# Optimization experiments

Measured on AMD Instinct MI355X. Metric: run time of the kernel, lower is better.

## Reference

```python
import jax, jax.numpy as jnp
import numpy as np

EPSILON = 1e-8
MATCH_THRESHOLD = 0.5
MEANINGFUL_RADIUS = 0.05


def setup_inputs() -> dict:
    key = jax.random.key(0)
    ks = jax.random.split(key, 8)
    B, T, H, D, N = 4, 4096, 2048, 256, 8192
    K = H // 4
    s = lambda k, shape, fan_in: jax.random.normal(k, shape, jnp.float32) * (fan_in ** -0.5)
    return {
        "hidden": jax.random.normal(ks[0], (B, T, H), jnp.float32),
        "beliefs": jax.random.normal(ks[1], (N, D), jnp.float32),
        "active_mask": jax.random.bernoulli(ks[2], 0.9, (N,)),
        "W_obs": s(ks[3], (D, H), H),
        "W_g1": s(ks[4], (K, H), H),
        "b_g1": jnp.zeros((K,), jnp.float32),
        "W_g2": s(ks[5], (1, K), K),
        "b_g2": jnp.full((1,), -2.0, jnp.float32),  # nn.init.constant_(bias, -2.0)
        "W_p1": s(ks[6], (K, H), H),
        "b_p1": jnp.zeros((K,), jnp.float32),
        "W_p2": s(ks[7], (1, K), K),
        "b_p2": jnp.zeros((1,), jnp.float32),
    }


def reference(hidden, beliefs, active_mask, W_obs, W_g1, b_g1, W_g2, b_g2, W_p1, b_p1, W_p2, b_p2):
    # --- projections over [B, T, H] ---
    obs = jnp.einsum('bth,dh->btd', hidden, W_obs)                       # [B,T,D]
    g_h = jax.nn.relu(jnp.einsum('bth,kh->btk', hidden, W_g1) + b_g1)
    gate = jax.nn.sigmoid(jnp.einsum('btk,ok->bto', g_h, W_g2) + b_g2)   # [B,T,1]
    p_h = jax.nn.relu(jnp.einsum('bth,kh->btk', hidden, W_p1) + b_p1)
    prec = jax.nn.softplus(jnp.einsum('btk,ok->bto', p_h, W_p2) + b_p2)  # [B,T,1]

    obs_mean = obs.mean(axis=0)            # [T,D]
    prec_mean = (gate * prec).mean(axis=0)  # [T,1]

    # F.normalize(x, dim=-1, eps) == x / max(||x||, eps)
    obs_angles = obs_mean / jnp.maximum(
        jnp.linalg.norm(obs_mean, axis=-1, keepdims=True), EPSILON)
    obs_beliefs = obs_angles * prec_mean    # [T,D], radius = gated precision

    # --- match against active belief slots (fully vectorized, no per-token loop) ---
    obs_r = jnp.linalg.norm(obs_beliefs, axis=-1)                       # [T]
    obs_ang = obs_beliefs / jnp.maximum(obs_r, EPSILON)[:, None]
    bel_r = jnp.maximum(jnp.linalg.norm(beliefs, axis=-1), EPSILON)     # [N]
    bel_ang = beliefs / bel_r[:, None]

    sims = obs_ang @ bel_ang.T              # [T,N] cosine similarities
    neg = jnp.finfo(sims.dtype).min
    masked = jnp.where(active_mask[None, :], sims, neg)
    any_active = jnp.any(active_mask)
    best_sims = jnp.where(any_active, masked.max(axis=-1), 0.0)         # [T]
    best_idx = jnp.where(any_active, jnp.argmax(masked, axis=-1), -1)   # [T]

    meaningful = obs_r > MEANINGFUL_RADIUS
    matched = meaningful & (best_sims > MATCH_THRESHOLD)
    matched_slot = jnp.where(matched, best_idx, -1)                     # -1 == new slot
    match_sim = jnp.where(matched, best_sims, 0.0)

    # vectorized stand-in for list[WriteCandidate]:
    # belief vectors, per-token match similarity, matched slot id, validity mask
    return obs_beliefs, match_sim, matched_slot, meaningful
```

## Files before the change

### kernel.cpp

```cpp
#include <hip/hip_runtime.h>

constexpr int B = 4, T = 4096, H = 2048, D = 256, KK = 512, N = 8192;
constexpr int BT = B * T;
constexpr int NALL = 1280;
constexpr int CAP = 1024;
constexpr int MCAP = 256;

typedef short bf16x8 __attribute__((ext_vector_type(8)));
typedef float f32x4  __attribute__((ext_vector_type(4)));

__device__ __forceinline__ unsigned short f2bf(float f) {
    unsigned u = __float_as_uint(f);
    return (unsigned short)((u + 0x7fffu + ((u >> 16) & 1u)) >> 16);
}
__device__ __forceinline__ float bf2f(unsigned short h) {
    return __uint_as_float((unsigned)h << 16);
}
__device__ __forceinline__ void async16(const void* g, void* l) {
    __builtin_amdgcn_global_load_lds(
        (const __attribute__((address_space(1))) unsigned int*)g,
        (__attribute__((address_space(3))) unsigned int*)l, 16, 0, 0);
}
__device__ __forceinline__ unsigned long long enc_sim(float s, int idx) {
    unsigned bits = __float_as_uint(s);
    unsigned e32 = (bits & 0x80000000u) ? ~bits : (bits | 0x80000000u);
    return ((unsigned long long)e32 << 32) | (unsigned)(~(unsigned)idx);
}
__device__ __forceinline__ unsigned enc_f32(float s) {
    unsigned b = __float_as_uint(s);
    return (b & 0x80000000u) ? ~b : (b | 0x80000000u);
}
__device__ __forceinline__ float dec_f32(unsigned e) {
    return __uint_as_float((e & 0x80000000u) ? (e & 0x7FFFFFFFu) : ~e);
}

constexpr size_t WS_HB   = 0;
constexpr size_t WS_WB   = WS_HB   + (size_t)BT * H * 2;
constexpr size_t WS_BELB = WS_WB   + (size_t)NALL * H * 2;
constexpr size_t WS_OAB  = WS_BELB + (size_t)N * D * 2;
constexpr size_t WS_B1C  = WS_OAB  + (size_t)T * D * 2;
constexpr size_t WS_W2C  = WS_B1C  + 4096;
constexpr size_t WS_FAC  = WS_W2C  + 4096;
constexpr size_t WS_OBSR = WS_FAC  + 16384;
constexpr size_t WS_FLAG = WS_OBSR + 16384;
constexpr size_t WS_ACTV = WS_FLAG + (size_t)CAP * 4;
constexpr size_t WS_META = WS_ACTV + (size_t)N * 4;
constexpr size_t WS_OBS  = WS_META + 256;
constexpr size_t WS_YG   = WS_OBS  + (size_t)T * D * 4;
constexpr size_t WS_YP   = WS_YG   + (size_t)BT * 4;
constexpr size_t WS_ENC  = WS_YP   + (size_t)BT * 4;
constexpr size_t WS_CNT  = WS_ENC  + (size_t)T * 4;
constexpr size_t WS_MCNT = WS_CNT  + 256;
constexpr size_t WS_MLST = WS_MCNT + 256;
constexpr size_t WS_ZEND = WS_MLST + (size_t)MCAP * 4;
constexpr size_t WS_NEEDF = WS_ZEND;
constexpr size_t WS_ZEROSZ = WS_ZEND - WS_OBS;

constexpr int    WTC    = 1280;
constexpr size_t F_WT   = 0;
constexpr size_t F_BEL  = F_WT   + (size_t)H * WTC * 4;
constexpr size_t F_OBS  = F_BEL  + (size_t)N * D * 4;
constexpr size_t F_YG   = F_OBS  + (size_t)T * D * 4;
constexpr size_t F_YP   = F_YG   + (size_t)BT * 4;
constexpr size_t F_OBSR = F_YP   + (size_t)BT * 4;
constexpr size_t F_ENC  = F_OBSR + (size_t)T * 4;
constexpr size_t F_ACT  = F_ENC  + (size_t)T * 8;
constexpr size_t F_META = F_ACT  + (size_t)N * 4;
constexpr size_t F_NEED = F_META + 256;

__global__ void prep_kernel(const float* beliefs, unsigned short* belb,
                            const unsigned char* mask_raw, int* active, int* meta,
                            const float* b_g1, const float* b_p1,
                            const float* W_g2, const float* W_p2,
                            float* b1c, float* w2c) {
    __shared__ int s_f32bad, s_nz_nonaligned;
    int blk = blockIdx.x;
    if (blk < N / 4) {
        int wave = blk * 4 + (threadIdx.x >> 6);
        int lane = threadIdx.x & 63;
        float4 v = ((const float4*)(beliefs + (size_t)wave * D))[lane];
        float ss = v.x * v.x + v.y * v.y + v.z * v.z + v.w * v.w;
        for (int m = 1; m < 64; m <<= 1) ss += __shfl_xor(ss, m, 64);
        float inv = 1.0f / fmaxf(sqrtf(ss), 1e-8f);
        uint2 o;
        o.x = f2bf(v.x * inv) | ((unsigned)f2bf(v.y * inv) << 16);
        o.y = f2bf(v.z * inv) | ((unsigned)f2bf(v.w * inv) << 16);
        *(uint2*)(belb + (size_t)wave * D + lane * 4) = o;
        return;
    }
    if (blk == N / 4) {
        if (threadIdx.x == 0) { s_f32bad = 0; s_nz_nonaligned = 0; }
        __syncthreads();
        const float* rf = (const float*)mask_raw;
        const int*   ri = (const int*)mask_raw;
        for (int i = threadIdx.x; i < N; i += blockDim.x) {
            unsigned char b = mask_raw[i];
            if ((i & 3) && b) atomicOr(&s_nz_nonaligned, 1);
        }
        for (int e = threadIdx.x; e < N / 4; e += blockDim.x) {
            float f = rf[e]; if (!(f == 0.0f || f == 1.0f)) atomicOr(&s_f32bad, 1);
        }
        __syncthreads();
        int layout;
        if (!s_f32bad)            layout = 2;
        else if (s_nz_nonaligned) layout = 1;
        else                      layout = 0;
        for (int n = threadIdx.x; n < N; n += blockDim.x) {
            int a;
            if (layout == 2)      a = (rf[n] != 0.0f);
            else if (layout == 1) a = (mask_raw[n] != 0);
            else                  a = (ri[n] != 0);
            active[n] = a;
        }
        if (threadIdx.x == 0) meta[0] = layout;
        return;
    }
    for (int c = threadIdx.x; c < 1024; c += blockDim.x) {
        if (c < 512) { b1c[c] = b_g1[c];       w2c[c] = W_g2[c]; }
        else         { b1c[c] = b_p1[c - 512]; w2c[c] = W_p2[c - 512]; }
    }
}

__global__ void conv_all(const float* hidden, const float* Wg1, const float* Wp1,
                         const float* Wobs, unsigned short* hb, unsigned short* wb) {
    int blk = blockIdx.x;
    int c8 = threadIdx.x * 8;
    const float* src;
    unsigned short* dst;
    if (blk < BT) {
        src = hidden + (size_t)blk * H;
        dst = hb + (size_t)blk * H;
    } else {
        int row = blk - BT;
        src = (row < 512) ? &Wg1[(size_t)row * H]
            : (row < 1024) ? &Wp1[(size_t)(row - 512) * H]
                           : &Wobs[(size_t)(row - 1024) * H];
        dst = wb + (size_t)row * H;
    }
    float4 v0 = *(const float4*)(src + c8);
    float4 v1 = *(const float4*)(src + c8 + 4);
    uint4 o;
    o.x = f2bf(v0.x) | ((unsigned)f2bf(v0.y) << 16);
    o.y = f2bf(v0.z) | ((unsigned)f2bf(v0.w) << 16);
    o.z = f2bf(v1.x) | ((unsigned)f2bf(v1.y) << 16);
    o.w = f2bf(v1.z) | ((unsigned)f2bf(v1.w) << 16);
    *(uint4*)(dst + c8) = o;
}

__global__ __launch_bounds__(256) void big_gemm(const unsigned short* Ab, const unsigned short* Bb,
                                                const float* b1c, const float* w2c,
                                                float* yg, float* yp, float* obs_buf) {
    __shared__ unsigned short As[128 * 32];
    __shared__ unsigned short Bs[128 * 32];
    __shared__ float b1s[128], w2s[128];
    int tid = threadIdx.x;
    int mb = blockIdx.x, nb = blockIdx.y;
    int m0 = mb * 128, n0 = nb * 128;
    bool is_mlp = (nb < 8);
    if (is_mlp && tid < 128) { b1s[tid] = b1c[n0 + tid]; w2s[tid] = w2c[n0 + tid]; }
    int wave = tid >> 6, lane = tid & 63;
    int wr = wave >> 1, wc = wave & 1;
    int quad = lane >> 4, mrow = lane & 15;
    f32x4 acc[4][4] = {};
    const unsigned short* gA = Ab + (size_t)(m0 + (tid >> 2)) * H + (tid & 3) * 8;
    const unsigned short* gB = Bb + (size_t)(n0 + (tid >> 2)) * H + (tid & 3) * 8;
    char* lA = (char*)As + wave * 1024;
    char* lB = (char*)Bs + wave * 1024;
    for (int k0 = 0; k0 < H; k0 += 32) {
        async16(gA + k0, lA);
        async16(gA + (size_t)64 * H + k0, lA + 4096);
        async16(gB + k0, lB);
        async16(gB + (size_t)64 * H + k0, lB + 4096);
        __syncthreads();
        bf16x8 a[4], b[4];
        for (int i = 0; i < 4; i++) a[i] = *(const bf16x8*)&As[(wr * 64 + i * 16 + mrow) * 32 + quad * 8];
        for (int j = 0; j < 4; j++) b[j] = *(const bf16x8*)&Bs[(wc * 64 + j * 16 + mrow) * 32 + quad * 8];
        for (int i = 0; i < 4; i++)
            for (int j = 0; j < 4; j++)
                acc[i][j] = __builtin_amdgcn_mfma_f32_16x16x32_bf16(a[i], b[j], acc[i][j], 0, 0, 0);
        __syncthreads();
    }
    if (is_mlp) {
        float* y = (nb < 4) ? yg : yp;
        for (int i = 0; i < 4; i++) {
            int row_g = m0 + wr * 64 + i * 16 + quad * 4;
            for (int r = 0; r < 4; r++) {
                float s = 0.0f;
                for (int j = 0; j < 4; j++) {
                    int cl = wc * 64 + j * 16 + mrow;
                    float z = fmaxf(acc[i][j][r] + b1s[cl], 0.0f);
                    s += z * w2s[cl];
                }
                s += __shfl_xor(s, 1); s += __shfl_xor(s, 2);
                s += __shfl_xor(s, 4); s += __shfl_xor(s, 8);
                if (mrow == 0) atomicAdd(&y[row_g + r], s);
            }
        }
    } else {
        for (int i = 0; i < 4; i++)
            for (int r = 0; r < 4; r++) {
                int row_g = m0 + wr * 64 + i * 16 + quad * 4 + r;
                int t = row_g & (T - 1);
                for (int j = 0; j < 4; j++) {
                    int d = n0 - 1024 + wc * 64 + j * 16 + mrow;
                    atomicAdd(&obs_buf[(size_t)t * D + d], acc[i][j][r] * 0.25f);
                }
            }
    }
}

__global__ void finalize_fast(const float* yg, const float* yp, const float* obs_buf,
                              const float* b_g2, const float* b_p2,
                              float* out0, float* out3, float* obs_r_ws, float* fac,
                              unsigned short* oab, int* flaglist, int* flagcnt,
                              float* yg_mut, float* yp_mut) {
    int t = blockIdx.x * 4 + (threadIdx.x >> 6);
    int lane = threadIdx.x & 63;
    if (t >= T) return;
    float bg2 = b_g2[0], bp2 = b_p2[0];
    float pm = 0.0f;
    for (int b = 0; b < B; ++b) {
        float g = yg[b * T + t] + bg2;
        float p = yp[b * T + t] + bp2;
        float gate = 1.0f / (1.0f + expf(-g));
        float prec = (p > 20.0f) ? p : log1pf(expf(p));
        pm += gate * prec;
    }
    pm *= 0.25f;
    float4 v = ((const float4*)(obs_buf + (size_t)t * D))[lane];
    float ss = v.x * v.x + v.y * v.y + v.z * v.z + v.w * v.w;
    for (int m = 1; m < 64; m <<= 1) ss += __shfl_xor(ss, m, 64);
    float norm = sqrtf(ss);
    float na = fmaxf(norm, 1e-8f);
    float f = norm / na;
    float inv = 1.0f / na;
    float ax = v.x * inv, ay = v.y * inv, az = v.z * inv, aw = v.w * inv;
    float4 ob; ob.x = ax * pm; ob.y = ay * pm; ob.z = az * pm; ob.w = aw * pm;
    ((float4*)(out0 + (size_t)t * D))[lane] = ob;
    uint2 oa;
    oa.x = f2bf(ax) | ((unsigned)f2bf(ay) << 16);
    oa.y = f2bf(az) | ((unsigned)f2bf(aw) << 16);
    *(uint2*)(oab + (size_t)t * D + lane * 4) = oa;
    if (lane == 0) {
        float obs_r = pm * f;
        obs_r_ws[t] = obs_r;
        fac[t] = f;
        out3[t] = (obs_r > 0.05f) ? 1.0f : 0.0f;
        if (fabsf(obs_r - 0.05f) < 5.0e-4f) {
            int idx = atomicAdd(flagcnt, 1);
            if (idx < CAP) {
                flaglist[idx] = t;
                for (int b = 0; b < B; ++b) { yg_mut[b * T + t] = 0.0f; yp_mut[b * T + t] = 0.0f; }
            }
        }
    }
}

__global__ __launch_bounds__(256) void refine_mfma(const float* hidden,
        const float* W_g1, const float* W_p1, const float* b1c, const float* w2c,
        const int* flaglist, const int* flagcnt, float* yg, float* yp) {
    int nrows = min(*flagcnt, CAP) * 4;
    int m0 = blockIdx.x * 64;
    if (m0 >= nrows) return;
    int nb = blockIdx.y;
    int n0 = nb * 128;
    __shared__ unsigned short Ahi[64 * 32], Alo[64 * 32];
    __shared__ unsigned short Bhi[128 * 32], Blo[128 * 32];
    __shared__ int rowg_s[64];
    __shared__ float b1s[128], w2s[128];
    int tid = threadIdx.x;
    if (tid < 64) {
        int fr = m0 + tid;
        int rg = -1;
        if (fr < nrows) { int tok = flaglist[fr >> 2]; rg = (fr & 3) * T + tok; }
        rowg_s[tid] = rg;
    } else if (tid >= 128) {
        int c = tid - 128;
        b1s[c] = b1c[n0 + c]; w2s[c] = w2c[n0 + c];
    }
    __syncthreads();
    const float* Wbase = (n0 < 512) ? W_g1 : W_p1;
    int wofs = n0 & 511;
    int arow = tid >> 2, kseg = (tid & 3) * 8;
    int argr = rowg_s[arow]; if (argr < 0) argr = 0;
    const float* aptr = hidden + (size_t)argr * H + kseg;
    const float* bptr0 = Wbase + (size_t)(wofs + arow) * H + kseg;
    const float* bptr1 = Wbase + (size_t)(wofs + arow + 64) * H + kseg;
    int wave = tid >> 6, lane = tid & 63;
    int quad = lane >> 4, mrow = lane & 15;
    f32x4 acc[4][2] = {};
    for (int k0 = 0; k0 < H; k0 += 32) {
        float xs[8];
        {
            float4 v0 = *(const float4*)(aptr + k0);
            float4 v1 = *(const float4*)(aptr + k0 + 4);
            xs[0]=v0.x; xs[1]=v0.y; xs[2]=v0.z; xs[3]=v0.w;
            xs[4]=v1.x; xs[5]=v1.y; xs[6]=v1.z; xs[7]=v1.w;
            unsigned short hi[8], lo[8];
            for (int q = 0; q < 8; q++) {
                hi[q] = f2bf(xs[q]);
                lo[q] = f2bf(xs[q] - bf2f(hi[q]));
            }
            uint4 ph, pl;
            ph.x = hi[0]|((unsigned)hi[1]<<16); ph.y = hi[2]|((unsigned)hi[3]<<16);
            ph.z = hi[4]|((unsigned)hi[5]<<16); ph.w = hi[6]|((unsigned)hi[7]<<16);
            pl.x = lo[0]|((unsigned)lo[1]<<16); pl.y = lo[2]|((unsigned)lo[3]<<16);
            pl.z = lo[4]|((unsigned)lo[5]<<16); pl.w = lo[6]|((unsigned)lo[7]<<16);
            *(uint4*)&Ahi[arow * 32 + kseg] = ph;
            *(uint4*)&Alo[arow * 32 + kseg] = pl;
        }
        for (int half = 0; half < 2; half++) {
            const float* bp = half ? bptr1 : bptr0;
            float4 v0 = *(const float4*)(bp + k0);
            float4 v1 = *(const float4*)(bp + k0 + 4);
            xs[0]=v0.x; xs[1]=v0.y; xs[2]=v0.z; xs[3]=v0.w;
            xs[4]=v1.x; xs[5]=v1.y; xs[6]=v1.z; xs[7]=v1.w;
            unsigned short hi[8], lo[8];
            for (int q = 0; q < 8; q++) {
                hi[q] = f2bf(xs[q]);
                lo[q] = f2bf(xs[q] - bf2f(hi[q]));
            }
            uint4 ph, pl;
            ph.x = hi[0]|((unsigned)hi[1]<<16); ph.y = hi[2]|((unsigned)hi[3]<<16);
            ph.z = hi[4]|((unsigned)hi[5]<<16); ph.w = hi[6]|((unsigned)hi[7]<<16);
            pl.x = lo[0]|((unsigned)lo[1]<<16); pl.y = lo[2]|((unsigned)lo[3]<<16);
            pl.z = lo[4]|((unsigned)lo[5]<<16); pl.w = lo[6]|((unsigned)lo[7]<<16);
            *(uint4*)&Bhi[(arow + half * 64) * 32 + kseg] = ph;
            *(uint4*)&Blo[(arow + half * 64) * 32 + kseg] = pl;
        }
        __syncthreads();
        bf16x8 ah[4], al[4], bh[2], bl[2];
        for (int i = 0; i < 4; i++) {
            ah[i] = *(const bf16x8*)&Ahi[(i * 16 + mrow) * 32 + quad * 8];
            al[i] = *(const bf16x8*)&Alo[(i * 16 + mrow) * 32 + quad * 8];
        }
        for (int j = 0; j < 2; j++) {
            bh[j] = *(const bf16x8*)&Bhi[(wave * 32 + j * 16 + mrow) * 32 + quad * 8];
            bl[j] = *(const bf16x8*)&Blo[(wave * 32 + j * 16 + mrow) * 32 + quad * 8];
        }
        for (int i = 0; i < 4; i++)
            for (int j = 0; j < 2; j++) {
                acc[i][j] = __builtin_amdgcn_mfma_f32_16x16x32_bf16(al[i], bh[j], acc[i][j], 0, 0, 0);
                acc[i][j] = __builtin_amdgcn_mfma_f32_16x16x32_bf16(ah[i], bl[j], acc[i][j], 0, 0, 0);
                acc[i][j] = __builtin_amdgcn_mfma_f32_16x16x32_bf16(ah[i], bh[j], acc[i][j], 0, 0, 0);
            }
        __syncthreads();
    }
    float* y = (nb < 4) ? yg : yp;
    for (int i = 0; i < 4; i++)
        for (int r = 0; r < 4; r++) {
            int row_l = i * 16 + quad * 4 + r;
            float s = 0.0f;
            for (int j = 0; j < 2; j++) {
                int cl = wave * 32 + j * 16 + mrow;
                float z = fmaxf(acc[i][j][r] + b1s[cl], 0.0f);
                s += z * w2s[cl];
            }
            s += __shfl_xor(s, 1); s += __shfl_xor(s, 2);
            s += __shfl_xor(s, 4); s += __shfl_xor(s, 8);
            if (mrow == 0) {
                int rg = rowg_s[row_l];
                if (rg >= 0) atomicAdd(&y[rg], s);
            }
        }
}

__global__ void refine_pm(const float* yg, const float* yp, const float* b_g2, const float* b_p2,
                          const int* flagcnt, const int* flaglist, const float* fac,
                          float* obs_r_ws, float* out3) {
    int nflag = min(*flagcnt, CAP);
    int idx = blockIdx.x * 64 + threadIdx.x;
    if (idx >= nflag) return;
    int t = flaglist[idx];
    float bg2 = b_g2[0], bp2 = b_p2[0];
    float pm = 0.0f;
    for (int b = 0; b < B; ++b) {
        float g = yg[b * T + t] + bg2;
        float p = yp[b * T + t] + bp2;
        float gate = 1.0f / (1.0f + expf(-g));
        float prec = (p > 20.0f) ? p : log1pf(expf(p));
        pm += gate * prec;
    }
    pm *= 0.25f;
    float obs_r = pm * fac[t];
    obs_r_ws[t] = obs_r;
    out3[t] = (obs_r > 0.05f) ? 1.0f : 0.0f;
}

__global__ __launch_bounds__(256) void sims_mfma(const unsigned short* oab, const unsigned short* belb,
                                                 const int* active, unsigned* encg) {
    __shared__ unsigned short As[128 * 32];
    __shared__ unsigned short Bs[128 * 32];
    __shared__ int acts[128];
    int tid = threadIdx.x;
    int mb = blockIdx.x, nb = blockIdx.y;
    int m0 = mb * 128, n0 = nb * 128;
    if (tid < 128) acts[tid] = active[n0 + tid];
    int wave = tid >> 6, lane = tid & 63;
    int wr = wave >> 1, wc = wave & 1;
    int quad = lane >> 4, mrow = lane & 15;
    f32x4 acc[4][4] = {};
    const unsigned short* gA = oab + (size_t)(m0 + (tid >> 2)) * D + (tid & 3) * 8;
    const unsigned short* gB = belb + (size_t)(n0 + (tid >> 2)) * D + (tid & 3) * 8;
    char* lA = (char*)As + wave * 1024;
    char* lB = (char*)Bs + wave * 1024;
    for (int k0 = 0; k0 < D; k0 += 32) {
        async16(gA + k0, lA);
        async16(gA + (size_t)64 * D + k0, lA + 4096);
        async16(gB + k0, lB);
        async16(gB + (size_t)64 * D + k0, lB + 4096);
        __syncthreads();
        bf16x8 a[4], b[4];
        for (int i = 0; i < 4; i++) a[i] = *(const bf16x8*)&As[(wr * 64 + i * 16 + mrow) * 32 + quad * 8];
        for (int j = 0; j < 4; j++) b[j] = *(const bf16x8*)&Bs[(wc * 64 + j * 16 + mrow) * 32 + quad * 8];
        for (int i = 0; i < 4; i++)
            for (int j = 0; j < 4; j++)
                acc[i][j] = __builtin_amdgcn_mfma_f32_16x16x32_bf16(a[i], b[j], acc[i][j], 0, 0, 0);
        __syncthreads();
    }
    for (int i = 0; i < 4; i++)
        for (int r = 0; r < 4; r++) {
            int row_g = m0 + wr * 64 + i * 16 + quad * 4 + r;
            float m = -3.4e38f;
            for (int j = 0; j < 4; j++) {
                int cl = wc * 64 + j * 16 + mrow;
                if (acts[cl]) m = fmaxf(m, acc[i][j][r]);
            }
            m = fmaxf(m, __shfl_xor(m, 1)); m = fmaxf(m, __shfl_xor(m, 2));
            m = fmaxf(m, __shfl_xor(m, 4)); m = fmaxf(m, __shfl_xor(m, 8));
            if (mrow == 0 && m > 0.45f) atomicMax(&encg[row_g], enc_f32(m));
        }
}

__global__ void outw_kernel(const unsigned* encg, const float* obs_r_ws,
                            float* out1, float* out2, int* mcnt, int* mlist) {
    int t = blockIdx.x * 256 + threadIdx.x;
    if (t >= T) return;
    unsigned ev = encg[t];
    float best = (ev == 0u) ? -3.4e38f : dec_f32(ev);
    bool meaningful = obs_r_ws[t] > 0.05f;
    bool matched = meaningful && (best > 0.5f);
    out1[t] = matched ? best : 0.0f;
    out2[t] = -1.0f;
    if (matched) {
        int slot = atomicAdd(mcnt, 1);
        if (slot < MCAP) mlist[slot] = t;
    }
}

__global__ void argmax_kernel(const unsigned short* oab, const unsigned short* belb,
                              const int* active, const int* mcnt, const int* mlist,
                              float* out1, float* out2) {
    int nm = min(*mcnt, MCAP);
    int j = blockIdx.x;
    if (j >= nm) return;
    int t = mlist[j];
    __shared__ float q[256];
    __shared__ unsigned long long red[256];
    if (threadIdx.x < 128) {
        unsigned v = ((const unsigned*)(oab + (size_t)t * D))[threadIdx.x];
        q[threadIdx.x * 2]     = bf2f((unsigned short)(v & 0xFFFF));
        q[threadIdx.x * 2 + 1] = bf2f((unsigned short)(v >> 16));
    }
    __syncthreads();
    float best = -3.4e38f; int bi = -1;
    for (int k = 0; k < N / 256; k++) {
        int n = threadIdx.x + k * 256;
        if (!active[n]) continue;
        const uint4* br = (const uint4*)(belb + (size_t)n * D);
        float s = 0.0f;
        for (int c = 0; c < 32; c++) {
            uint4 v = br[c];
            const unsigned* pv = (const unsigned*)&v;
            for (int w = 0; w < 4; w++) {
                s += q[c * 8 + w * 2]     * bf2f((unsigned short)(pv[w] & 0xFFFF));
                s += q[c * 8 + w * 2 + 1] * bf2f((unsigned short)(pv[w] >> 16));
            }
        }
        if (s > best) { best = s; bi = n; }
    }
    red[threadIdx.x] = (bi >= 0) ? enc_sim(best, bi) : 0ULL;
    __syncthreads();
    for (int st = 128; st > 0; st >>= 1) {
        if (threadIdx.x < st) red[threadIdx.x] = max(red[threadIdx.x], red[threadIdx.x + st]);
        __syncthreads();
    }
    if (threadIdx.x == 0) {
        unsigned long long ev = red[0];
        if (ev) {
            unsigned e32 = (unsigned)(ev >> 32);
            out1[t] = __uint_as_float((e32 & 0x80000000u) ? (e32 & 0x7FFFFFFFu) : ~e32);
            out2[t] = (float)(int)~((unsigned)(ev & 0xFFFFFFFFu));
        }
    }
}

__global__ void f_mask_kernel(const unsigned char* raw, int* active, int* meta) {
    __shared__ int s_f32bad, s_nz_nonaligned;
    if (threadIdx.x == 0) { s_f32bad = 0; s_nz_nonaligned = 0; }
    __syncthreads();
    const float* rf = (const float*)raw;
    const int*   ri = (const int*)raw;
    for (int i = threadIdx.x; i < N; i += blockDim.x) {
        unsigned char b = raw[i];
        if ((i & 3) && b) atomicOr(&s_nz_nonaligned, 1);
    }
    for (int e = threadIdx.x; e < N / 4; e += blockDim.x) {
        float f = rf[e]; if (!(f == 0.0f || f == 1.0f)) atomicOr(&s_f32bad, 1);
    }
    __syncthreads();
    int layout = (!s_f32bad) ? 2 : (s_nz_nonaligned ? 1 : 0);
    for (int n = threadIdx.x; n < N; n += blockDim.x) {
        int a;
        if (layout == 2)      a = (rf[n] != 0.0f);
        else if (layout == 1) a = (raw[n] != 0);
        else                  a = (ri[n] != 0);
        active[n] = a;
    }
    if (threadIdx.x == 0) meta[0] = layout;
}

__global__ void wt_kernel(const float* Wg1, const float* Wp1, const float* Wobs, float* WT) {
    __shared__ float tile[32][33];
    int hb = blockIdx.x * 32, cb = blockIdx.y * 32;
    int x = threadIdx.x & 31, y = threadIdx.x >> 5;
    for (int i = 0; i < 32; i += 8) {
        int c = cb + y + i;
        const float* src = (c < 512) ? &Wg1[(size_t)c * H]
                         : (c < 1024) ? &Wp1[(size_t)(c - 512) * H]
                                      : &Wobs[(size_t)(c - 1024) * H];
        tile[y + i][x] = src[hb + x];
    }
    __syncthreads();
    for (int i = 0; i < 32; i += 8)
        WT[(size_t)(hb + y + i) * WTC + cb + x] = tile[x][y + i];
}

__global__ void belprep_kernel(const float* beliefs, float* bel_ang) {
    int wave = (blockIdx.x * blockDim.x + threadIdx.x) >> 6;
    int lane = threadIdx.x & 63;
    if (wave >= N) return;
    float4 v = ((const float4*)(beliefs + (size_t)wave * D))[lane];
    float ss = v.x * v.x + v.y * v.y + v.z * v.z + v.w * v.w;
    for (int m = 1; m < 64; m <<= 1) ss += __shfl_xor(ss, m, 64);
    float inv = 1.0f / fmaxf(sqrtf(ss), 1e-8f);
    float4 o; o.x = v.x * inv; o.y = v.y * inv; o.z = v.z * inv; o.w = v.w * inv;
    ((float4*)(bel_ang + (size_t)wave * D))[lane] = o;
}

__global__ __launch_bounds__(256) void gemm_obs_kernel(const float* hidden, const float* WT,
                                                       float* obs_mean) {
    __shared__ float As[32][33];
    __shared__ float Ws[32][260];
    int t0 = blockIdx.x * 32;
    int tx = threadIdx.x & 63, ty = threadIdx.x >> 6;
    float acc[8][4] = {};
    for (int h0 = 0; h0 < H; h0 += 32) {
        for (int q = 0; q < 4; ++q) {
            int e = threadIdx.x + q * 256;
            int r = e >> 5, kk = e & 31;
            float s = 0.0f;
            for (int b = 0; b < B; ++b) s += hidden[((size_t)b * T + t0 + r) * H + h0 + kk];
            As[kk][r] = s;
        }
        for (int q = 0; q < 8; ++q) {
            int e4 = threadIdx.x + q * 256;
            int kk = e4 >> 6, c4 = (e4 & 63) * 4;
            *(float4*)&Ws[kk][c4] = *(const float4*)&WT[(size_t)(h0 + kk) * WTC + 1024 + c4];
        }
        __syncthreads();
        for (int kk = 0; kk < 32; ++kk) {
            float a[8], w[4];
            for (int i = 0; i < 8; i++) a[i] = As[kk][ty * 8 + i];
            for (int j = 0; j < 4; j++) w[j] = Ws[kk][tx + 64 * j];
            for (int i = 0; i < 8; i++)
                for (int j = 0; j < 4; j++) acc[i][j] += a[i] * w[j];
        }
        __syncthreads();
    }
    for (int i = 0; i < 8; i++)
        for (int j = 0; j < 4; j++)
            obs_mean[(size_t)(t0 + ty * 8 + i) * D + tx + 64 * j] = acc[i][j] * 0.25f;
}

__global__ __launch_bounds__(512, 4) void gemm_mlp_kernel(
        const float* hidden, const float* WT,
        const float* b1g, const float* b1p, const float* w2g, const float* w2p,
        const float* b2g, const float* b2p, float* yg, float* yp) {
    __shared__ float As[16][65];
    __shared__ float Ws[16][516];
    int R = blockIdx.x * 64;
    int path = blockIdx.y;
    int cbase = path * 512;
    int tx = threadIdx.x & 63, ty = threadIdx.x >> 6;
    float acc[8][8] = {};
    for (int h0 = 0; h0 < H; h0 += 16) {
        {   int r = threadIdx.x >> 3, k2 = (threadIdx.x & 7) * 2;
            float2 v = *(const float2*)&hidden[(size_t)(R + r) * H + h0 + k2];
            As[k2][r] = v.x; As[k2 + 1][r] = v.y; }
        for (int q = 0; q < 4; ++q) {
            int e4 = threadIdx.x + q * 512;
            int kk = e4 >> 7, c4 = (e4 & 127) * 4;
            *(float4*)&Ws[kk][c4] = *(const float4*)&WT[(size_t)(h0 + kk) * WTC + cbase + c4];
        }
        __syncthreads();
        for (int kk = 0; kk < 16; ++kk) {
            float a[8], w[8];
            for (int i = 0; i < 8; i++) a[i] = As[kk][ty * 8 + i];
            for (int j = 0; j < 8; j++) w[j] = Ws[kk][tx + 64 * j];
            for (int i = 0; i < 8; i++)
                for (int j = 0; j < 8; j++) acc[i][j] += a[i] * w[j];
        }
        __syncthreads();
    }
    const float* b1 = path ? b1p : b1g;
    const float* w2 = path ? w2p : w2g;
    float b2 = path ? b2p[0] : b2g[0];
    float part[8];
    for (int i = 0; i < 8; i++) {
        float s = 0.0f;
        for (int j = 0; j < 8; j++) {
            int c = tx + 64 * j;
            float z = fmaxf(acc[i][j] + b1[c], 0.0f);
            s += z * w2[c];
        }
        part[i] = s;
    }
    for (int m = 1; m < 64; m <<= 1)
        for (int i = 0; i < 8; i++) part[i] += __shfl_xor(part[i], m, 64);
    if (tx == 0) {
        float* dst = path ? yp : yg;
        for (int i = 0; i < 8; i++) dst[R + ty * 8 + i] = part[i] + b2;
    }
}

__global__ void finalize_kernel(const float* yg, const float* yp, float* obs,
                                float* out0, float* out3, float* obs_r_ws,
                                unsigned long long* enc) {
    int t = blockIdx.x * 4 + (threadIdx.x >> 6);
    int lane = threadIdx.x & 63;
    if (t >= T) return;
    float pm = 0.0f;
    for (int b = 0; b < B; ++b) {
        float g = yg[b * T + t], p = yp[b * T + t];
        float gate = 1.0f / (1.0f + expf(-g));
        float prec = (p > 15.0f) ? p : log1pf(expf(p));
        pm += gate * prec;
    }
    pm *= (1.0f / B);
    float4 v = ((const float4*)(obs + (size_t)t * D))[lane];
    float ss = v.x * v.x + v.y * v.y + v.z * v.z + v.w * v.w;
    for (int m = 1; m < 64; m <<= 1) ss += __shfl_xor(ss, m, 64);
    float norm = sqrtf(ss);
    float na = fmaxf(norm, 1e-8f);
    float4 ob;
    ob.x = v.x / na * pm; ob.y = v.y / na * pm;
    ob.z = v.z / na * pm; ob.w = v.w / na * pm;
    float obs_r = pm * (norm / na);
    ((float4*)(out0 + (size_t)t * D))[lane] = ob;
    float ra = fmaxf(obs_r, 1e-8f);
    float4 oa;
    oa.x = ob.x / ra; oa.y = ob.y / ra; oa.z = ob.z / ra; oa.w = ob.w / ra;
    ((float4*)(obs + (size_t)t * D))[lane] = oa;
    if (lane == 0) {
        out3[t] = (obs_r > 0.05f) ? 1.0f : 0.0f;
        obs_r_ws[t] = obs_r;
        enc[t] = 0ULL;
    }
}

__global__ __launch_bounds__(256) void sims_kernel(const float* obs_ang, const float* bel_ang,
                                                   const int* active, unsigned long long* enc) {
    __shared__ float Aos[64][68];
    __shared__ float Bbs[64][68];
    __shared__ unsigned long long lmax[64];
    __shared__ int act[64];
    int tb = blockIdx.x * 64, nb = blockIdx.y * 64;
    int tx = threadIdx.x & 15, ty = threadIdx.x >> 4;
    if (threadIdx.x < 64) { lmax[threadIdx.x] = 0ULL; act[threadIdx.x] = active[nb + threadIdx.x]; }
    float acc[4][4] = {};
    for (int d0 = 0; d0 < D; d0 += 64) {
        for (int q = 0; q < 4; ++q) {
            int e4 = threadIdx.x + q * 256;
            int r = e4 >> 4, c4 = (e4 & 15) * 4;
            *(float4*)&Aos[r][c4] = *(const float4*)&obs_ang[(size_t)(tb + r) * D + d0 + c4];
            *(float4*)&Bbs[r][c4] = *(const float4*)&bel_ang[(size_t)(nb + r) * D + d0 + c4];
        }
        __syncthreads();
        for (int dd = 0; dd < 64; ++dd) {
            float a[4], w[4];
            for (int i = 0; i < 4; i++) a[i] = Aos[ty + 16 * i][dd];
            for (int j = 0; j < 4; j++) w[j] = Bbs[tx + 16 * j][dd];
            for (int i = 0; i < 4; i++)
                for (int j = 0; j < 4; j++) acc[i][j] += a[i] * w[j];
        }
        __syncthreads();
    }
    for (int i = 0; i < 4; i++) {
        unsigned long long best = 0ULL;
        for (int j = 0; j < 4; j++) {
            int c = tx + 16 * j;
            if (act[c]) {
                unsigned long long ev = enc_sim(acc[i][j], nb + c);
                if (ev > best) best = ev;
            }
        }
        atomicMax(&lmax[ty + 16 * i], best);
    }
    __syncthreads();
    if (threadIdx.x < 64 && lmax[threadIdx.x])
        atomicMax(&enc[tb + threadIdx.x], lmax[threadIdx.x]);
}

__global__ void f_outw_kernel(const unsigned long long* enc, const float* obs_r_ws,
                              float* out1, float* out2) {
    int t = blockIdx.x * 256 + threadIdx.x;
    if (t >= T) return;
    unsigned long long ev = enc[t];
    float best; int idx;
    if (ev == 0ULL) { best = -3.4e38f; idx = -1; }
    else {
        unsigned int e32 = (unsigned int)(ev >> 32);
        unsigned int bits = (e32 & 0x80000000u) ? (e32 & 0x7FFFFFFFu) : ~e32;
        best = __uint_as_float(bits);
        idx = (int)~((unsigned int)(ev & 0xFFFFFFFFu));
    }
    bool meaningful = obs_r_ws[t] > 0.05f;
    bool matched = meaningful && (best > 0.5f);
    out1[t] = matched ? best : 0.0f;
    out2[t] = matched ? (float)idx : -1.0f;
}

extern "C" void kernel_launch(void* const* d_in, const int* in_sizes, int n_in,
                              void* d_out, int out_size, void* d_ws, size_t ws_size,
                              hipStream_t stream) {
    const float* hidden  = (const float*)d_in[0];
    const float* beliefs = (const float*)d_in[1];
    const unsigned char* mask_raw = (const unsigned char*)d_in[2];
    const float* W_obs = (const float*)d_in[3];
    const float* W_g1  = (const float*)d_in[4];
    const float* b_g1  = (const float*)d_in[5];
    const float* W_g2  = (const float*)d_in[6];
    const float* b_g2  = (const float*)d_in[7];
    const float* W_p1  = (const float*)d_in[8];
    const float* b_p1  = (const float*)d_in[9];
    const float* W_p2  = (const float*)d_in[10];
    const float* b_p2  = (const float*)d_in[11];

    float* out0 = (float*)d_out;
    float* out1 = out0 + (size_t)T * D;
    float* out2 = out1 + T;
    float* out3 = out2 + T;
    char* ws = (char*)d_ws;

    if (ws_size >= WS_NEEDF) {
        unsigned short* hb   = (unsigned short*)(ws + WS_HB);
        unsigned short* wb   = (unsigned short*)(ws + WS_WB);
        unsigned short* belb = (unsigned short*)(ws + WS_BELB);
        unsigned short* oab  = (unsigned short*)(ws + WS_OAB);
        float* b1c     = (float*)(ws + WS_B1C);
        float* w2c     = (float*)(ws + WS_W2C);
        float* fac     = (float*)(ws + WS_FAC);
        float* obs_r   = (float*)(ws + WS_OBSR);
        int*   flaglist= (int*)(ws + WS_FLAG);
        int*   active  = (int*)(ws + WS_ACTV);
        int*   meta    = (int*)(ws + WS_META);
        float* obs_buf = (float*)(ws + WS_OBS);
        float* yg      = (float*)(ws + WS_YG);
        float* yp      = (float*)(ws + WS_YP);
        unsigned* encg = (unsigned*)(ws + WS_ENC);
        int*   flagcnt = (int*)(ws + WS_CNT);
        int*   mcnt    = (int*)(ws + WS_MCNT);
        int*   mlist   = (int*)(ws + WS_MLST);

        hipMemsetAsync(ws + WS_OBS, 0, WS_ZEROSZ, stream);
        prep_kernel<<<N / 4 + 2, 256, 0, stream>>>(beliefs, belb, mask_raw, active, meta,
                                                   b_g1, b_p1, W_g2, W_p2, b1c, w2c);
        conv_all<<<BT + NALL, 256, 0, stream>>>(hidden, W_g1, W_p1, W_obs, hb, wb);
        big_gemm<<<dim3(BT / 128, NALL / 128), 256, 0, stream>>>(hb, wb, b1c, w2c, yg, yp, obs_buf);
        finalize_fast<<<T / 4, 256, 0, stream>>>(yg, yp, obs_buf, b_g2, b_p2,
                                                 out0, out3, obs_r, fac, oab,
                                                 flaglist, flagcnt, yg, yp);
        refine_mfma<<<dim3(CAP * 4 / 64, 8), 256, 0, stream>>>(hidden, W_g1, W_p1, b1c, w2c,
                                                               flaglist, flagcnt, yg, yp);
        refine_pm<<<CAP / 64, 64, 0, stream>>>(yg, yp, b_g2, b_p2, flagcnt, flaglist,
                                               fac, obs_r, out3);
        sims_mfma<<<dim3(T / 128, N / 128), 256, 0, stream>>>(oab, belb, active, encg);
        outw_kernel<<<(T + 255) / 256, 256, 0, stream>>>(encg, obs_r, out1, out2, mcnt, mlist);
        argmax_kernel<<<MCAP, 256, 0, stream>>>(oab, belb, active, mcnt, mlist, out1, out2);
        return;
    }

    if (ws_size < F_NEED) return;
    float* WT       = (float*)(ws + F_WT);
    float* bel_ang  = (float*)(ws + F_BEL);
    float* obs_buf  = (float*)(ws + F_OBS);
    float* yg       = (float*)(ws + F_YG);
    float* yp       = (float*)(ws + F_YP);
    float* obs_r_ws = (float*)(ws + F_OBSR);
    unsigned long long* enc = (unsigned long long*)(ws + F_ENC);
    int* active     = (int*)(ws + F_ACT);
    int* meta       = (int*)(ws + F_META);

    f_mask_kernel<<<1, 1024, 0, stream>>>(mask_raw, active, meta);
    wt_kernel<<<dim3(H / 32, WTC / 32), 256, 0, stream>>>(W_g1, W_p1, W_obs, WT);
    belprep_kernel<<<N / 4, 256, 0, stream>>>(beliefs, bel_ang);
    gemm_obs_kernel<<<T / 32, 256, 0, stream>>>(hidden, WT, obs_buf);
    gemm_mlp_kernel<<<dim3(BT / 64, 2), 512, 0, stream>>>(
        hidden, WT, b_g1, b_p1, W_g2, W_p2, b_g2, b_p2, yg, yp);
    finalize_kernel<<<T / 4, 256, 0, stream>>>(yg, yp, obs_buf, out0, out3, obs_r_ws, enc);
    sims_kernel<<<dim3(T / 64, N / 64), 256, 0, stream>>>(obs_buf, bel_ang, active, enc);
    f_outw_kernel<<<(T + 255) / 256, 256, 0, stream>>>(enc, obs_r_ws, out1, out2);
}
```

Before: 500.1 us.

## Fuse prep, conversion and zeroing kernels; fold refine_pm into outw; halve refine tile

Merges the memset, prep and bf16 conversion launches into one prep_conv kernel whose extra blocks zero the workspace. The per-token precision/meaningful computation from refine_pm moves into outw_kernel, which removes one launch and the obs_r workspace buffer. refine_mfma now uses 64-column tiles over twice as many grid columns to raise parallelism for the small flagged-row GEMM. This cuts launch overhead and serialization between small kernels, at the cost of recomputing gate/prec for every token instead of only the flagged ones.

New measurement: 500.9 us. Within noise of the previous version (+0.2%).

```diff
diff --git a/kernel.cpp b/kernel.cpp
--- a/kernel.cpp
+++ b/kernel.cpp
@@ -55,6 +55,14 @@
 constexpr size_t WS_ZEND = WS_MLST + (size_t)MCAP * 4;
 constexpr size_t WS_NEEDF = WS_ZEND;
 constexpr size_t WS_ZEROSZ = WS_ZEND - WS_OBS;
+constexpr int NZB = (int)((WS_ZEROSZ + 4095) / 4096);
+
+constexpr int PC_CONV = BT + NALL;
+constexpr int PC_BEL  = PC_CONV + N / 4;
+constexpr int PC_MASK = PC_BEL;
+constexpr int PC_VEC  = PC_MASK + 1;
+constexpr int PC_ZERO = PC_VEC + 1;
+constexpr int PC_GRID = PC_ZERO + NZB;
 
 constexpr int    WTC    = 1280;
 constexpr size_t F_WT   = 0;
@@ -68,15 +76,41 @@
 constexpr size_t F_META = F_ACT  + (size_t)N * 4;
 constexpr size_t F_NEED = F_META + 256;
 
-__global__ void prep_kernel(const float* beliefs, unsigned short* belb,
-                            const unsigned char* mask_raw, int* active, int* meta,
-                            const float* b_g1, const float* b_p1,
-                            const float* W_g2, const float* W_p2,
-                            float* b1c, float* w2c) {
+__global__ void prep_conv(const float* hidden, const float* Wg1, const float* Wp1,
+                          const float* Wobs, unsigned short* hb, unsigned short* wb,
+                          const float* beliefs, unsigned short* belb,
+                          const unsigned char* mask_raw, int* active, int* meta,
+                          const float* b_g1, const float* b_p1,
+                          const float* W_g2, const float* W_p2,
+                          float* b1c, float* w2c, char* zbase) {
     __shared__ int s_f32bad, s_nz_nonaligned;
     int blk = blockIdx.x;
-    if (blk < N / 4) {
-        int wave = blk * 4 + (threadIdx.x >> 6);
+    if (blk < PC_CONV) {
+        int c8 = threadIdx.x * 8;
+        const float* src;
+        unsigned short* dst;
+        if (blk < BT) {
+            src = hidden + (size_t)blk * H;
+            dst = hb + (size_t)blk * H;
+        } else {
+            int row = blk - BT;
+            src = (row < 512) ? &Wg1[(size_t)row * H]
+                : (row < 1024) ? &Wp1[(size_t)(row - 512) * H]
+                               : &Wobs[(size_t)(row - 1024) * H];
+            dst = wb + (size_t)row * H;
+        }
+        float4 v0 = *(const float4*)(src + c8);
+        float4 v1 = *(const float4*)(src + c8 + 4);
+        uint4 o;
+        o.x = f2bf(v0.x) | ((unsigned)f2bf(v0.y) << 16);
+        o.y = f2bf(v0.z) | ((unsigned)f2bf(v0.w) << 16);
+        o.z = f2bf(v1.x) | ((unsigned)f2bf(v1.y) << 16);
+        o.w = f2bf(v1.z) | ((unsigned)f2bf(v1.w) << 16);
+        *(uint4*)(dst + c8) = o;
+        return;
+    }
+    if (blk < PC_BEL) {
+        int wave = (blk - PC_CONV) * 4 + (threadIdx.x >> 6);
         int lane = threadIdx.x & 63;
         float4 v = ((const float4*)(beliefs + (size_t)wave * D))[lane];
         float ss = v.x * v.x + v.y * v.y + v.z * v.z + v.w * v.w;
@@ -88,7 +122,7 @@
         *(uint2*)(belb + (size_t)wave * D + lane * 4) = o;
         return;
     }
-    if (blk == N / 4) {
+    if (blk == PC_MASK) {
         if (threadIdx.x == 0) { s_f32bad = 0; s_nz_nonaligned = 0; }
         __syncthreads();
         const float* rf = (const float*)mask_raw;
@@ -115,36 +149,18 @@
         if (threadIdx.x == 0) meta[0] = layout;
         return;
     }
-    for (int c = threadIdx.x; c < 1024; c += blockDim.x) {
-        if (c < 512) { b1c[c] = b_g1[c];       w2c[c] = W_g2[c]; }
-        else         { b1c[c] = b_p1[c - 512]; w2c[c] = W_p2[c - 512]; }
-    }
-}
-
-__global__ void conv_all(const float* hidden, const float* Wg1, const float* Wp1,
-                         const float* Wobs, unsigned short* hb, unsigned short* wb) {
-    int blk = blockIdx.x;
-    int c8 = threadIdx.x * 8;
-    const float* src;
-    unsigned short* dst;
-    if (blk < BT) {
-        src = hidden + (size_t)blk * H;
-        dst = hb + (size_t)blk * H;
-    } else {
-        int row = blk - BT;
-        src = (row < 512) ? &Wg1[(size_t)row * H]
-            : (row < 1024) ? &Wp1[(size_t)(row - 512) * H]
-                           : &Wobs[(size_t)(row - 1024) * H];
-        dst = wb + (size_t)row * H;
-    }
-    float4 v0 = *(const float4*)(src + c8);
-    float4 v1 = *(const float4*)(src + c8 + 4);
-    uint4 o;
-    o.x = f2bf(v0.x) | ((unsigned)f2bf(v0.y) << 16);
-    o.y = f2bf(v0.z) | ((unsigned)f2bf(v0.w) << 16);
-    o.z = f2bf(v1.x) | ((unsigned)f2bf(v1.y) << 16);
-    o.w = f2bf(v1.z) | ((unsigned)f2bf(v1.w) << 16);
-    *(uint4*)(dst + c8) = o;
+    if (blk == PC_VEC) {
+        for (int c = threadIdx.x; c < 1024; c += blockDim.x) {
+            if (c < 512) { b1c[c] = b_g1[c];       w2c[c] = W_g2[c]; }
+            else         { b1c[c] = b_p1[c - 512]; w2c[c] = W_p2[c - 512]; }
+        }
+        return;
+    }
+    size_t off = (size_t)(blk - PC_ZERO) * 4096 + (size_t)threadIdx.x * 16;
+    if (off + 16 <= WS_ZEROSZ) {
+        uint4 z = {0u, 0u, 0u, 0u};
+        *(uint4*)(zbase + off) = z;
+    }
 }
 
 __global__ __launch_bounds__(256) void big_gemm(const unsigned short* Ab, const unsigned short* Bb,
@@ -211,7 +227,7 @@
 
 __global__ void finalize_fast(const float* yg, const float* yp, const float* obs_buf,
                               const float* b_g2, const float* b_p2,
-                              float* out0, float* out3, float* obs_r_ws, float* fac,
+                              float* out0, float* out3, float* fac,
                               unsigned short* oab, int* flaglist, int* flagcnt,
                               float* yg_mut, float* yp_mut) {
     int t = blockIdx.x * 4 + (threadIdx.x >> 6);
@@ -243,7 +259,6 @@
     *(uint2*)(oab + (size_t)t * D + lane * 4) = oa;
     if (lane == 0) {
         float obs_r = pm * f;
-        obs_r_ws[t] = obs_r;
         fac[t] = f;
         out3[t] = (obs_r > 0.05f) ? 1.0f : 0.0f;
         if (fabsf(obs_r - 0.05f) < 5.0e-4f) {
@@ -263,18 +278,18 @@
     int m0 = blockIdx.x * 64;
     if (m0 >= nrows) return;
     int nb = blockIdx.y;
-    int n0 = nb * 128;
+    int n0 = nb * 64;
     __shared__ unsigned short Ahi[64 * 32], Alo[64 * 32];
-    __shared__ unsigned short Bhi[128 * 32], Blo[128 * 32];
+    __shared__ unsigned short Bhi[64 * 32], Blo[64 * 32];
     __shared__ int rowg_s[64];
-    __shared__ float b1s[128], w2s[128];
+    __shared__ float b1s[64], w2s[64];
     int tid = threadIdx.x;
     if (tid < 64) {
         int fr = m0 + tid;
         int rg = -1;
         if (fr < nrows) { int tok = flaglist[fr >> 2]; rg = (fr & 3) * T + tok; }
         rowg_s[tid] = rg;
-    } else if (tid >= 128) {
+    } else if (tid >= 128 && tid < 192) {
         int c = tid - 128;
         b1s[c] = b1c[n0 + c]; w2s[c] = w2c[n0 + c];
     }
@@ -284,11 +299,10 @@
     int arow = tid >> 2, kseg = (tid & 3) * 8;
     int argr = rowg_s[arow]; if (argr < 0) argr = 0;
     const float* aptr = hidden + (size_t)argr * H + kseg;
-    const float* bptr0 = Wbase + (size_t)(wofs + arow) * H + kseg;
-    const float* bptr1 = Wbase + (size_t)(wofs + arow + 64) * H + kseg;
+    const float* bptr = Wbase + (size_t)(wofs + arow) * H + kseg;
     int wave = tid >> 6, lane = tid & 63;
     int quad = lane >> 4, mrow = lane & 15;
-    f32x4 acc[4][2] = {};
+    f32x4 acc[4] = {};
     for (int k0 = 0; k0 < H; k0 += 32) {
         float xs[8];
         {
@@ -309,10 +323,9 @@
             *(uint4*)&Ahi[arow * 32 + kseg] = ph;
             *(uint4*)&Alo[arow * 32 + kseg] = pl;
         }
-        for (int half = 0; half < 2; half++) {
-            const float* bp = half ? bptr1 : bptr0;
-            float4 v0 = *(const float4*)(bp + k0);
-            float4 v1 = *(const float4*)(bp + k0 + 4);
+        {
+            float4 v0 = *(const float4*)(bptr + k0);
+            float4 v1 = *(const float4*)(bptr + k0 + 4);
             xs[0]=v0.x; xs[1]=v0.y; xs[2]=v0.z; xs[3]=v0.w;
             xs[4]=v1.x; xs[5]=v1.y; xs[6]=v1.z; xs[7]=v1.w;
             unsigned short hi[8], lo[8];
@@ -325,37 +338,31 @@
             ph.z = hi[4]|((unsigned)hi[5]<<16); ph.w = hi[6]|((unsigned)hi[7]<<16);
             pl.x = lo[0]|((unsigned)lo[1]<<16); pl.y = lo[2]|((unsigned)lo[3]<<16);
             pl.z = lo[4]|((unsigned)lo[5]<<16); pl.w = lo[6]|((unsigned)lo[7]<<16);
-            *(uint4*)&Bhi[(arow + half * 64) * 32 + kseg] = ph;
-            *(uint4*)&Blo[(arow + half * 64) * 32 + kseg] = pl;
-        }
-        __syncthreads();
-        bf16x8 ah[4], al[4], bh[2], bl[2];
+            *(uint4*)&Bhi[arow * 32 + kseg] = ph;
+            *(uint4*)&Blo[arow * 32 + kseg] = pl;
+        }
+        __syncthreads();
+        bf16x8 ah[4], al[4], bh, bl;
         for (int i = 0; i < 4; i++) {
             ah[i] = *(const bf16x8*)&Ahi[(i * 16 + mrow) * 32 + quad * 8];
             al[i] = *(const bf16x8*)&Alo[(i * 16 + mrow) * 32 + quad * 8];
         }
-        for (int j = 0; j < 2; j++) {
-            bh[j] = *(const bf16x8*)&Bhi[(wave * 32 + j * 16 + mrow) * 32 + quad * 8];
-            bl[j] = *(const bf16x8*)&Blo[(wave * 32 + j * 16 + mrow) * 32 + quad * 8];
-        }
-        for (int i = 0; i < 4; i++)
-            for (int j = 0; j < 2; j++) {
-                acc[i][j] = __builtin_amdgcn_mfma_f32_16x16x32_bf16(al[i], bh[j], acc[i][j], 0, 0, 0);
-                acc[i][j] = __builtin_amdgcn_mfma_f32_16x16x32_bf16(ah[i], bl[j], acc[i][j], 0, 0, 0);
-                acc[i][j] = __builtin_amdgcn_mfma_f32_16x16x32_bf16(ah[i], bh[j], acc[i][j], 0, 0, 0);
-            }
-        __syncthreads();
-    }
-    float* y = (nb < 4) ? yg : yp;
+        bh = *(const bf16x8*)&Bhi[(wave * 16 + mrow) * 32 + quad * 8];
+        bl = *(const bf16x8*)&Blo[(wave * 16 + mrow) * 32 + quad * 8];
+        for (int i = 0; i < 4; i++) {
+            acc[i] = __builtin_amdgcn_mfma_f32_16x16x32_bf16(al[i], bh, acc[i], 0, 0, 0);
+            acc[i] = __builtin_amdgcn_mfma_f32_16x16x32_bf16(ah[i], bl, acc[i], 0, 0, 0);
+            acc[i] = __builtin_amdgcn_mfma_f32_16x16x32_bf16(ah[i], bh, acc[i], 0, 0, 0);
+        }
+        __syncthreads();
+    }
+    float* y = (nb < 8) ? yg : yp;
+    int cl = wave * 16 + mrow;
     for (int i = 0; i < 4; i++)
         for (int r = 0; r < 4; r++) {
             int row_l = i * 16 + quad * 4 + r;
-            float s = 0.0f;
-            for (int j = 0; j < 2; j++) {
-                int cl = wave * 32 + j * 16 + mrow;
-                float z = fmaxf(acc[i][j][r] + b1s[cl], 0.0f);
-                s += z * w2s[cl];
-            }
+            float z = fmaxf(acc[i][r] + b1s[cl], 0.0f);
+            float s = z * w2s[cl];
             s += __shfl_xor(s, 1); s += __shfl_xor(s, 2);
             s += __shfl_xor(s, 4); s += __shfl_xor(s, 8);
             if (mrow == 0) {
@@ -363,28 +370,6 @@
                 if (rg >= 0) atomicAdd(&y[rg], s);
             }
         }
-}
-
-__global__ void refine_pm(const float* yg, const float* yp, const float* b_g2, const float* b_p2,
-                          const int* flagcnt, const int* flaglist, const float* fac,
-                          float* obs_r_ws, float* out3) {
-    int nflag = min(*flagcnt, CAP);
-    int idx = blockIdx.x * 64 + threadIdx.x;
-    if (idx >= nflag) return;
-    int t = flaglist[idx];
-    float bg2 = b_g2[0], bp2 = b_p2[0];
-    float pm = 0.0f;
-    for (int b = 0; b < B; ++b) {
-        float g = yg[b * T + t] + bg2;
-        float p = yp[b * T + t] + bp2;
-        float gate = 1.0f / (1.0f + expf(-g));
-        float prec = (p > 20.0f) ? p : log1pf(expf(p));
-        pm += gate * prec;
-    }
-    pm *= 0.25f;
-    float obs_r = pm * fac[t];
-    obs_r_ws[t] = obs_r;
-    out3[t] = (obs_r > 0.05f) ? 1.0f : 0.0f;
 }
 
 __global__ __launch_bounds__(256) void sims_mfma(const unsigned short* oab, const unsigned short* belb,
@@ -432,13 +417,26 @@
         }
 }
 
-__global__ void outw_kernel(const unsigned* encg, const float* obs_r_ws,
-                            float* out1, float* out2, int* mcnt, int* mlist) {
+__global__ void outw_kernel(const unsigned* encg, const float* yg, const float* yp,
+                            const float* b_g2, const float* b_p2, const float* fac,
+                            float* out1, float* out2, float* out3, int* mcnt, int* mlist) {
     int t = blockIdx.x * 256 + threadIdx.x;
     if (t >= T) return;
+    float bg2 = b_g2[0], bp2 = b_p2[0];
+    float pm = 0.0f;
+    for (int b = 0; b < B; ++b) {
+        float g = yg[b * T + t] + bg2;
+        float p = yp[b * T + t] + bp2;
+        float gate = 1.0f / (1.0f + expf(-g));
+        float prec = (p > 20.0f) ? p : log1pf(expf(p));
+        pm += gate * prec;
+    }
+    pm *= 0.25f;
+    float obs_r = pm * fac[t];
+    bool meaningful = obs_r > 0.05f;
+    out3[t] = meaningful ? 1.0f : 0.0f;
     unsigned ev = encg[t];
     float best = (ev == 0u) ? -3.4e38f : dec_f32(ev);
-    bool meaningful = obs_r_ws[t] > 0.05f;
     bool matched = meaningful && (best > 0.5f);
     out1[t] = matched ? best : 0.0f;
     out2[t] = -1.0f;
@@ -761,7 +759,6 @@
         float* b1c     = (float*)(ws + WS_B1C);
         float* w2c     = (float*)(ws + WS_W2C);
         float* fac     = (float*)(ws + WS_FAC);
-        float* obs_r   = (float*)(ws + WS_OBSR);
         int*   flaglist= (int*)(ws + WS_FLAG);
         int*   active  = (int*)(ws + WS_ACTV);
         int*   meta    = (int*)(ws + WS_META);
@@ -773,20 +770,19 @@
         int*   mcnt    = (int*)(ws + WS_MCNT);
         int*   mlist   = (int*)(ws + WS_MLST);
 
-        hipMemsetAsync(ws + WS_OBS, 0, WS_ZEROSZ, stream);
-        prep_kernel<<<N / 4 + 2, 256, 0, stream>>>(beliefs, belb, mask_raw, active, meta,
-                                                   b_g1, b_p1, W_g2, W_p2, b1c, w2c);
-        conv_all<<<BT + NALL, 256, 0, stream>>>(hidden, W_g1, W_p1, W_obs, hb, wb);
+        prep_conv<<<PC_GRID, 256, 0, stream>>>(hidden, W_g1, W_p1, W_obs, hb, wb,
+                                               beliefs, belb, mask_raw, active, meta,
+                                               b_g1, b_p1, W_g2, W_p2, b1c, w2c,
+                                               ws + WS_OBS);
         big_gemm<<<dim3(BT / 128, NALL / 128), 256, 0, stream>>>(hb, wb, b1c, w2c, yg, yp, obs_buf);
         finalize_fast<<<T / 4, 256, 0, stream>>>(yg, yp, obs_buf, b_g2, b_p2,
-                                                 out0, out3, obs_r, fac, oab,
+                                                 out0, out3, fac, oab,
                                                  flaglist, flagcnt, yg, yp);
-        refine_mfma<<<dim3(CAP * 4 / 64, 8), 256, 0, stream>>>(hidden, W_g1, W_p1, b1c, w2c,
-                                                               flaglist, flagcnt, yg, yp);
-        refine_pm<<<CAP / 64, 64, 0, stream>>>(yg, yp, b_g2, b_p2, flagcnt, flaglist,
-                                               fac, obs_r, out3);
+        refine_mfma<<<dim3(CAP * 4 / 64, 16), 256, 0, stream>>>(hidden, W_g1, W_p1, b1c, w2c,
+                                                                flaglist, flagcnt, yg, yp);
         sims_mfma<<<dim3(T / 128, N / 128), 256, 0, stream>>>(oab, belb, active, encg);
-        outw_kernel<<<(T + 255) / 256, 256, 0, stream>>>(encg, obs_r, out1, out2, mcnt, mlist);
+        outw_kernel<<<(T + 255) / 256, 256, 0, stream>>>(encg, yg, yp, b_g2, b_p2, fac,
+                                                         out1, out2, out3, mcnt, mlist);
         argmax_kernel<<<MCAP, 256, 0, stream>>>(oab, belb, active, mcnt, mlist, out1, out2);
         return;
     }
```
